# Kernel optimization log

Hardware: AMD Instinct MI355X
Metric: run time of the kernel (lower is better)

The kernel has to match this reference:

```python
import jax, jax.numpy as jnp
import numpy as np
import math

B, N, NBS, E, H = 64, 512, 8, 2048, 128
L, K = 3, 4
AF, BF = 82, 6
NA, NBTAB = 100, 10
ALPHA, LAMDA = 0.1, 0.5


def _gelu(x):
    return jax.nn.gelu(x, approximate=False)


def _mask_softmax(a, mask):
    # a: [..., n], mask broadcastable to a; matches torch mask_softmax (eps=1e-6)
    a_exp = jnp.exp(a - jnp.max(a, -1, keepdims=True)) * mask
    return a_exp / (jnp.sum(a_exp, -1, keepdims=True) + 1e-6)


def _gru(x, h, wih, whh, bih, bhh):
    # torch.nn.GRUCell semantics; wih/whh: [3H, H] in (r, z, n) order
    gi = x @ wih.T + bih
    gh = h @ whh.T + bhh
    ir, iz, inn = jnp.split(gi, 3, -1)
    hr, hz, hn = jnp.split(gh, 3, -1)
    r = jax.nn.sigmoid(ir + hr)
    z = jax.nn.sigmoid(iz + hz)
    n = jnp.tanh(inn + r * hn)
    return (1 - z) * n + z * h


def setup_inputs() -> dict:
    key = jax.random.key(0)
    ks = iter(jax.random.split(key, 64))
    def nrm(shape, s=0.05):
        return jax.random.normal(next(ks), shape, dtype=jnp.float32) * s
    def zb(shape):
        return jnp.zeros(shape, jnp.float32)
    inp = dict(
        batch_size=B,
        vertex_mask=jnp.ones((B, N), jnp.float32),
        vertex=jax.random.randint(next(ks), (B, N), 0, NA),
        edge=jax.random.randint(next(ks), (B, E), 0, NBTAB),
        atom_adj=jax.random.randint(next(ks), (B, N, NBS), 0, B * N),
        bond_adj=jax.random.randint(next(ks), (B, N, NBS), 0, B * E),
        nbs_mask=jnp.ones((B, N, NBS), jnp.float32),
        init_atom_features=nrm((NA, AF), 1.0),
        init_bond_features=nrm((NBTAB, BF), 1.0),
        emb_w=nrm((AF, H)), emb_b=zb((H,)),
        u1_w=nrm((L, H + BF, H)), u1_b=zb((L, H)),
        u2_w=nrm((L, 2 * H, H)), u2_b=zb((L, H)),
        fu_w=nrm((L, H, H)), fu_b=zb((L, H)),
        wvm_w=nrm((L, K, H, H)), wvm_b=zb((L, K, H)),
        wmain_w=nrm((L, K, H, H)), wmain_b=zb((L, K, H)),
        wbmm_w=nrm((L, K, H)), wbmm_b=zb((L, K)),
        khead_w=nrm((L, K * H, H)), khead_b=zb((L, H)),
        wmaster_w=nrm((L, H, H)), wmaster_b=zb((L, H)),
        wm2m_w=nrm((L, H, H)), wm2m_b=zb((L, H)),
        wzm1_w=nrm((L, H, H)), wzm1_b=zb((L, H)),
        wzm2_w=nrm((L, H, H)), wzm2_b=zb((L, H)),
        wzs1_w=nrm((L, H, H)), wzs1_b=zb((L, H)),
        wzs2_w=nrm((L, H, H)), wzs2_b=zb((L, H)),
        gru_main_wih=nrm((3 * H, H)), gru_main_whh=nrm((3 * H, H)),
        gru_main_bih=zb((3 * H,)), gru_main_bhh=zb((3 * H,)),
        gru_master_wih=nrm((3 * H, H)), gru_master_whh=nrm((3 * H, H)),
        gru_master_bih=zb((3 * H,)), gru_master_bhh=zb((3 * H,)),
    )
    return inp


def _compute(p, vertex, edge, atom_adj, bond_adj):
    vm = p['vertex_mask']               # [B, N]
    nm = p['nbs_mask']                  # [B, N, NBS]
    b, n_vertex = vm.shape
    nbs = atom_adj.shape[-1]
    # embed initial atom/bond features via table gather
    v_init = p['init_atom_features'][vertex.reshape(-1)].reshape(b, n_vertex, -1)
    e_init = p['init_bond_features'][edge.reshape(-1)].reshape(b, edge.shape[1], -1)
    v_init = v_init * vm[:, :, None]
    vf = _gelu(v_init @ p['emb_w'] + p['emb_b'])                       # [B, N, H]
    h0 = vf
    hdim = vf.shape[-1]
    master = jnp.sum(vf * vm[:, :, None], axis=1, keepdims=True)        # [B, 1, H]
    aa = atom_adj.reshape(-1)
    ba = bond_adj.reshape(-1)
    n_layers = p['u1_w'].shape[0]
    for i in range(n_layers):
        # --- multi-head main -> master attention (all heads vectorized) ---
        mv = jnp.tanh(jnp.einsum('bnh,khd->bknd', vf, p['wvm_w'][i]) + p['wvm_b'][i][None, :, None, :])
        score = jnp.einsum('bknd,kd->bkn', mv * master[:, None, :, :], p['wbmm_w'][i]) + p['wbmm_b'][i][None, :, None]
        att = _mask_softmax(score, vm[:, None, :])                      # [B, K, N]
        proj = jnp.einsum('bnh,khd->bknd', vf, p['wmain_w'][i]) + p['wmain_b'][i][None, :, None, :]
        kmm = jnp.einsum('bkn,bknd->bkd', att, proj)                    # [B, K, H]
        main_to_master = jnp.tanh(kmm.reshape(b, 1, -1) @ p['khead_w'][i] + p['khead_b'][i])  # [B, 1, H]
        # --- GraphConvolution (dropout p = 0.0) ---
        vn = vf.reshape(-1, hdim)[aa].reshape(b, n_vertex, nbs, hdim)
        en = e_init.reshape(-1, e_init.shape[-1])[ba].reshape(b, n_vertex, nbs, -1)
        lab = _gelu(jnp.concatenate([vn, en], -1) @ p['u1_w'][i] + p['u1_b'][i])
        nl = jnp.sum(lab * nm[..., None], axis=-2)                      # [B, N, H]
        hi = jnp.concatenate([nl, vf], -1) @ p['u2_w'][i] + p['u2_b'][i]
        theta = math.log(LAMDA / (i + 1) + 1)
        support = (1 - ALPHA) * hi + ALPHA * h0
        self_vertex = theta * (support @ p['fu_w'][i] + p['fu_b'][i]) + (1 - theta) * support
        # --- master updates + gated mixing + GRU cells ---
        m2m = _gelu(master @ p['wm2m_w'][i] + p['wm2m_b'][i])           # [B, 1, H]
        mself = _gelu(master @ p['wmaster_w'][i] + p['wmaster_b'][i])   # [B, 1, H]
        z_main = jax.nn.sigmoid(self_vertex @ p['wzm1_w'][i] + p['wzm1_b'][i] + m2m @ p['wzm2_w'][i] + p['wzm2_b'][i])
        hidden_main = (1 - z_main) * self_vertex + z_main * m2m          # broadcast [B,N,H]
        vf = _gru(hidden_main.reshape(-1, hdim), vf.reshape(-1, hdim),
                  p['gru_main_wih'], p['gru_main_whh'], p['gru_main_bih'], p['gru_main_bhh']).reshape(b, n_vertex, hdim)
        z_master = jax.nn.sigmoid(mself @ p['wzs1_w'][i] + p['wzs1_b'][i] + main_to_master @ p['wzs2_w'][i] + p['wzs2_b'][i])
        hidden_super = (1 - z_master) * mself + z_master * main_to_master
        master = _gru(hidden_super.reshape(b, hdim), master.reshape(b, hdim),
                      p['gru_master_wih'], p['gru_master_whh'], p['gru_master_bih'], p['gru_master_bhh']).reshape(b, 1, hdim)
    return vf, master


def reference(batch_size, vertex_mask, vertex, edge, atom_adj, bond_adj, nbs_mask,
              init_atom_features, init_bond_features, emb_w, emb_b,
              u1_w, u1_b, u2_w, u2_b, fu_w, fu_b,
              wvm_w, wvm_b, wmain_w, wmain_b, wbmm_w, wbmm_b, khead_w, khead_b,
              wmaster_w, wmaster_b, wm2m_w, wm2m_b,
              wzm1_w, wzm1_b, wzm2_w, wzm2_b, wzs1_w, wzs1_b, wzs2_w, wzs2_b,
              gru_main_wih, gru_main_whh, gru_main_bih, gru_main_bhh,
              gru_master_wih, gru_master_whh, gru_master_bih, gru_master_bhh):
    p = dict(vertex_mask=vertex_mask, nbs_mask=nbs_mask,
             init_atom_features=init_atom_features, init_bond_features=init_bond_features,
             emb_w=emb_w, emb_b=emb_b, u1_w=u1_w, u1_b=u1_b, u2_w=u2_w, u2_b=u2_b,
             fu_w=fu_w, fu_b=fu_b, wvm_w=wvm_w, wvm_b=wvm_b, wmain_w=wmain_w, wmain_b=wmain_b,
             wbmm_w=wbmm_w, wbmm_b=wbmm_b, khead_w=khead_w, khead_b=khead_b,
             wmaster_w=wmaster_w, wmaster_b=wmaster_b, wm2m_w=wm2m_w, wm2m_b=wm2m_b,
             wzm1_w=wzm1_w, wzm1_b=wzm1_b, wzm2_w=wzm2_w, wzm2_b=wzm2_b,
             wzs1_w=wzs1_w, wzs1_b=wzs1_b, wzs2_w=wzs2_w, wzs2_b=wzs2_b,
             gru_main_wih=gru_main_wih, gru_main_whh=gru_main_whh,
             gru_main_bih=gru_main_bih, gru_main_bhh=gru_main_bhh,
             gru_master_wih=gru_master_wih, gru_master_whh=gru_master_whh,
             gru_master_bih=gru_master_bih, gru_master_bhh=gru_master_bhh)
    return _compute(p, vertex, edge, atom_adj, bond_adj)
```

## Files before the change

kernel.cpp:

```cpp
#include <hip/hip_runtime.h>
#include <hip/hip_bf16.h>
#include <cmath>

#define BB 64
#define NN 512
#define NBS 8
#define EE 2048
#define HH 128
#define LL 3
#define KK 4
#define AF 82
#define BF 6
#define SLAB 4194304

typedef __attribute__((ext_vector_type(8))) short bf16x8;
typedef __attribute__((ext_vector_type(4))) float f32x4;

__device__ __forceinline__ float gelu1(float x){ return 0.5f*x*(1.f+erff(x*0.7071067811865475f)); }
__device__ __forceinline__ float sig1(float x){ return 1.f/(1.f+expf(-x)); }
__device__ __forceinline__ short f2bs(float x){ __hip_bfloat16 b=__float2bfloat16(x); return *reinterpret_cast<short*>(&b); }
__device__ __forceinline__ float bs2f(short s){ unsigned u = ((unsigned)(unsigned short)s) << 16; union{unsigned u; float f;} c; c.u=u; return c.f; }
__device__ __forceinline__ void split2(float v, short& hi, short& lo){ hi = f2bs(v); lo = f2bs(v - bs2f(hi)); }

#define MFMA3(ACC, AH, AL, BH, BL) \
    ACC = __builtin_amdgcn_mfma_f32_16x16x32_bf16(AH, BH, ACC, 0,0,0); \
    ACC = __builtin_amdgcn_mfma_f32_16x16x32_bf16(AL, BH, ACC, 0,0,0); \
    ACC = __builtin_amdgcn_mfma_f32_16x16x32_bf16(AH, BL, ACC, 0,0,0);

__global__ __launch_bounds__(256) void layer_k1(
    const short* __restrict__ vfh, const short* __restrict__ vfl,
    const short* __restrict__ wtpv, short* __restrict__ pvfb,
    const short* __restrict__ wtwvm, const float* __restrict__ wvmb,
    const float* __restrict__ master,
    const float* __restrict__ wbw, const float* __restrict__ wbb,
    float* __restrict__ score)
{
    const int bid = blockIdx.x;
    const int t = threadIdx.x;
    const int lane = t & 63, wv = t >> 6;
    const int quad = lane >> 4, ml = lane & 15;

    if (bid < 256) {
        const int m0 = bid*128 + wv*32;
        const int r0 = m0 + ml, r1 = r0 + 16;

        bf16x8 a0h[4], a0l[4], a1h[4], a1l[4];
        #pragma unroll
        for (int kc = 0; kc < 4; ++kc) {
            const int kq = kc*32 + quad*8;
            a0h[kc] = *(const bf16x8*)(vfh + (size_t)r0*128 + kq);
            a0l[kc] = *(const bf16x8*)(vfl + (size_t)r0*128 + kq);
            a1h[kc] = *(const bf16x8*)(vfh + (size_t)r1*128 + kq);
            a1l[kc] = *(const bf16x8*)(vfl + (size_t)r1*128 + kq);
        }
        f32x4 acc[16];
        #pragma unroll
        for (int i = 0; i < 16; ++i) acc[i] = (f32x4){0.f,0.f,0.f,0.f};
        const short* wcol = wtpv + (size_t)ml*128;
        #pragma unroll
        for (int kc = 0; kc < 4; ++kc) {
            const int kq = kc*32 + quad*8;
            #pragma unroll
            for (int nt = 0; nt < 8; ++nt) {
                const short* bp = wcol + (size_t)nt*16*128 + kq;
                bf16x8 bh = *(const bf16x8*)bp;
                bf16x8 bl = *(const bf16x8*)(bp + 49152);
                MFMA3(acc[nt],   a0h[kc], a0l[kc], bh, bl);
                MFMA3(acc[8+nt], a1h[kc], a1l[kc], bh, bl);
            }
        }
        #pragma unroll
        for (int mt = 0; mt < 2; ++mt)
            #pragma unroll
            for (int nt = 0; nt < 8; ++nt) {
                int col = nt*16 + ml;
                #pragma unroll
                for (int r = 0; r < 4; ++r) {
                    int gm = m0 + mt*16 + quad*4 + r;
                    pvfb[(size_t)gm*128 + col] = f2bs(acc[mt*8+nt][r]);
                }
            }
    } else {
        const int v = bid - 256;
        const int k = v >> 8;
        const int tile = v & 255;
        const int b = tile >> 2;
        const int r0 = tile*128 + wv*32 + ml;
        const int r1 = r0 + 16;

        bf16x8 a0h[4], a0l[4], a1h[4], a1l[4];
        #pragma unroll
        for (int kc = 0; kc < 4; ++kc) {
            const int kq = kc*32 + quad*8;
            a0h[kc] = *(const bf16x8*)(vfh + (size_t)r0*128 + kq);
            a0l[kc] = *(const bf16x8*)(vfl + (size_t)r0*128 + kq);
            a1h[kc] = *(const bf16x8*)(vfh + (size_t)r1*128 + kq);
            a1l[kc] = *(const bf16x8*)(vfl + (size_t)r1*128 + kq);
        }
        f32x4 acc[16];
        #pragma unroll
        for (int i = 0; i < 16; ++i) acc[i] = (f32x4){0.f,0.f,0.f,0.f};
        const short* wcol = wtwvm + (size_t)k*16384 + (size_t)ml*128;
        #pragma unroll
        for (int kc = 0; kc < 4; ++kc) {
            const int kq = kc*32 + quad*8;
            #pragma unroll
            for (int nt = 0; nt < 8; ++nt) {
                const short* bp = wcol + (size_t)nt*16*128 + kq;
                bf16x8 bh = *(const bf16x8*)bp;
                bf16x8 bl = *(const bf16x8*)(bp + 196608);
                MFMA3(acc[nt],   a0h[kc], a0l[kc], bh, bl);
                MFMA3(acc[8+nt], a1h[kc], a1l[kc], bh, bl);
            }
        }
        float wv8[8], bj8[8];
        #pragma unroll
        for (int nt = 0; nt < 8; ++nt) {
            int col = nt*16 + ml;
            wv8[nt] = master[(size_t)b*128 + col] * wbw[(size_t)k*128 + col];
            bj8[nt] = wvmb[(size_t)k*128 + col];
        }
        float kb = wbb[k];
        #pragma unroll
        for (int mt = 0; mt < 2; ++mt) {
            #pragma unroll
            for (int r = 0; r < 4; ++r) {
                float s = 0.f;
                #pragma unroll
                for (int nt = 0; nt < 8; ++nt)
                    s += tanhf(acc[mt*8+nt][r] + bj8[nt]) * wv8[nt];
                s += __shfl_xor(s, 1); s += __shfl_xor(s, 2);
                s += __shfl_xor(s, 4); s += __shfl_xor(s, 8);
                if (ml == 0) {
                    int nloc = (tile & 3)*128 + wv*32 + mt*16 + quad*4 + r;
                    score[((size_t)(b*KK + k))*NN + nloc] = s + kb;
                }
            }
        }
    }
}

__global__ __launch_bounds__(256) void layer_k2(
    const short* __restrict__ pvfb, const float* __restrict__ pet,
    const int* __restrict__ aadj, const int* __restrict__ badj,
    const int* __restrict__ edge, const float* __restrict__ nbm,
    short* __restrict__ nlh, short* __restrict__ nll,
    const float* __restrict__ score, const float* __restrict__ vm,
    const float* __restrict__ vfc,
    float* __restrict__ satt, float* __restrict__ ctx)
{
    __shared__ float smem[768];
    const int bid = blockIdx.x;
    const int t = threadIdx.x;

    if (bid < 8192) {
        const int w = t >> 6, l = t & 63;
        const int i = bid*4 + w;
        const int sg = l >> 4, j = l & 15;
        float acc[8];
        #pragma unroll
        for (int c = 0; c < 8; ++c) acc[c] = 0.f;
        #pragma unroll
        for (int it = 0; it < 2; ++it) {
            int s = it*4 + sg;
            int flat = i*8 + s;
            int g = aadj[flat];
            int eid = edge[badj[flat]];
            float nv = nbm[flat];
            bf16x8 pv8 = *(const bf16x8*)(pvfb + (size_t)g*128 + j*8);
            const float* pp = pet + (size_t)eid*128 + j*8;
            float4 p0 = *(const float4*)pp, p1 = *(const float4*)(pp+4);
            float pe[8] = {p0.x,p0.y,p0.z,p0.w,p1.x,p1.y,p1.z,p1.w};
            #pragma unroll
            for (int c = 0; c < 8; ++c)
                acc[c] += gelu1(bs2f(pv8[c]) + pe[c]) * nv;
        }
        #pragma unroll
        for (int c = 0; c < 8; ++c) {
            acc[c] += __shfl_xor(acc[c], 16);
            acc[c] += __shfl_xor(acc[c], 32);
        }
        if (sg == 0) {
            short hs[8], ls[8];
            #pragma unroll
            for (int c = 0; c < 8; ++c) split2(acc[c], hs[c], ls[c]);
            size_t o = (size_t)i*128 + j*8;
            *(short4*)(nlh + o)     = make_short4(hs[0],hs[1],hs[2],hs[3]);
            *(short4*)(nlh + o + 4) = make_short4(hs[4],hs[5],hs[6],hs[7]);
            *(short4*)(nll + o)     = make_short4(ls[0],ls[1],ls[2],ls[3]);
            *(short4*)(nll + o + 4) = make_short4(ls[4],ls[5],ls[6],ls[7]);
        }
    } else {
        float* red = smem;
        float* att = smem + 256;
        const int bk = bid - 8192, b = bk >> 2;
        float v0 = score[(size_t)bk*NN + t], v1 = score[(size_t)bk*NN + 256 + t];
        red[t] = fmaxf(v0, v1); __syncthreads();
        for (int s = 128; s; s >>= 1) { if (t < s) red[t] = fmaxf(red[t], red[t+s]); __syncthreads(); }
        float mx = red[0]; __syncthreads();
        float e0 = expf(v0 - mx) * vm[b*NN + t];
        float e1 = expf(v1 - mx) * vm[b*NN + t + 256];
        red[t] = e0 + e1; __syncthreads();
        for (int s = 128; s; s >>= 1) { if (t < s) red[t] += red[t+s]; __syncthreads(); }
        float sum = red[0];
        float inv = 1.f / (sum + 1e-6f);
        att[t] = e0*inv; att[t+256] = e1*inv;
        if (t == 0) satt[bk] = sum*inv;
        __syncthreads();
        const int d = t & 127, h = t >> 7;
        float acc = 0.f;
        const float* V = vfc + (size_t)b*NN*HH;
        #pragma unroll 8
        for (int n = h*256; n < h*256 + 256; ++n) acc += att[n]*V[(size_t)n*HH + d];
        red[t] = acc; __syncthreads();
        if (t < 128) ctx[(size_t)bk*HH + t] = red[t] + red[t+128];
    }
}

__global__ __launch_bounds__(256, 2) void layer_k3(
    const short* __restrict__ nlh, const short* __restrict__ nll,
    const float* __restrict__ vfc, const short* __restrict__ vfch, const short* __restrict__ vfcl,
    float* __restrict__ vfn, short* __restrict__ vfnh, short* __restrict__ vfnl,
    const short* __restrict__ h0b,
    const short* __restrict__ wu2, const float* __restrict__ u2b,
    const short* __restrict__ wfu, const float* __restrict__ fub,
    const short* __restrict__ wzm, const float* __restrict__ zmb,
    const short* __restrict__ wih, const short* __restrict__ whh,
    const float* __restrict__ bih, const float* __restrict__ bhh,
    const float* __restrict__ t2, const float* __restrict__ m2m,
    float theta,
    const float* __restrict__ ctx, const float* __restrict__ satt,
    float* __restrict__ master,
    const float* __restrict__ wmain_w, const float* __restrict__ wmain_b,
    const float* __restrict__ khead_w, const float* __restrict__ khead_b,
    const float* __restrict__ wmaster_w, const float* __restrict__ wmaster_b,
    const float* __restrict__ wzs1_w,  const float* __restrict__ wzs1_b,
    const float* __restrict__ wzs2_w,  const float* __restrict__ wzs2_b,
    const float* __restrict__ WTih, const float* __restrict__ WThh,
    const float* __restrict__ bihm, const float* __restrict__ bhhm,
    const float* __restrict__ wm2m_n_w, const float* __restrict__ wm2m_n_b,
    const float* __restrict__ wzm2_n_w, const float* __restrict__ wzm2_n_b,
    float* __restrict__ m2m_out, float* __restrict__ t2_out)
{
    __shared__ __align__(16) char smem_raw[34816];
    const int bid = blockIdx.x;
    const int t = threadIdx.x;

    if (bid >= 64) {
        short* sh = (short*)smem_raw;
        short* sl = sh + 64*136;
        const int vb = bid - 64;
        const int lane = t & 63, wv = t >> 6;
        const int quad = lane >> 4, ml = lane & 15;
        const int base = vb * 64;
        const int bb = base >> 9;
        const int c0 = wv*32 + ml;
        const int c1 = c0 + 16;
        const int kq0 = quad*8;

        f32x4 acc[4][2];
        #pragma unroll
        for (int rt = 0; rt < 4; ++rt) {
            acc[rt][0] = (f32x4){0.f,0.f,0.f,0.f};
            acc[rt][1] = (f32x4){0.f,0.f,0.f,0.f};
        }

        #pragma unroll
        for (int kc = 0; kc < 4; ++kc) {
            const int kq = kc*32 + kq0;
            const short* bp0 = wu2 + (size_t)c0*256 + kq;
            const short* bp1 = wu2 + (size_t)c1*256 + kq;
            bf16x8 b0h = *(const bf16x8*)bp0, b0l = *(const bf16x8*)(bp0+98304);
            bf16x8 b1h = *(const bf16x8*)bp1, b1l = *(const bf16x8*)(bp1+98304);
            #pragma unroll
            for (int rt = 0; rt < 4; ++rt) {
                const size_t ar = (size_t)(base + rt*16 + ml);
                bf16x8 ah = *(const bf16x8*)(nlh + ar*128 + kq);
                bf16x8 al = *(const bf16x8*)(nll + ar*128 + kq);
                MFMA3(acc[rt][0], ah, al, b0h, b0l);
                MFMA3(acc[rt][1], ah, al, b1h, b1l);
            }
        }
        #pragma unroll
        for (int kc = 0; kc < 4; ++kc) {
            const int kq = kc*32 + kq0;
            const short* bp0 = wu2 + (size_t)c0*256 + 128 + kq;
            const short* bp1 = wu2 + (size_t)c1*256 + 128 + kq;
            bf16x8 b0h = *(const bf16x8*)bp0, b0l = *(const bf16x8*)(bp0+98304);
            bf16x8 b1h = *(const bf16x8*)bp1, b1l = *(const bf16x8*)(bp1+98304);
            #pragma unroll
            for (int rt = 0; rt < 4; ++rt) {
                const size_t ar = (size_t)(base + rt*16 + ml);
                bf16x8 ah = *(const bf16x8*)(vfch + ar*128 + kq);
                bf16x8 al = *(const bf16x8*)(vfcl + ar*128 + kq);
                MFMA3(acc[rt][0], ah, al, b0h, b0l);
                MFMA3(acc[rt][1], ah, al, b1h, b1l);
            }
        }
        f32x4 sup[4][2];
        {
            const float bj0 = u2b[c0], bj1 = u2b[c1];
            #pragma unroll
            for (int rt = 0; rt < 4; ++rt) {
                #pragma unroll
                for (int r = 0; r < 4; ++r) {
                    const size_t grow = (size_t)(base + rt*16 + quad*4 + r);
                    sup[rt][0][r] = 0.9f*(acc[rt][0][r]+bj0) + 0.1f*bs2f(h0b[grow*128 + c0]);
                    sup[rt][1][r] = 0.9f*(acc[rt][1][r]+bj1) + 0.1f*bs2f(h0b[grow*128 + c1]);
                    const int lrow = rt*16 + quad*4 + r;
                    short h_, l_;
                    split2(sup[rt][0][r], h_, l_); sh[lrow*136 + c0] = h_; sl[lrow*136 + c0] = l_;
                    split2(sup[rt][1][r], h_, l_); sh[lrow*136 + c1] = h_; sl[lrow*136 + c1] = l_;
                }
            }
        }
        __syncthreads();

        #pragma unroll
        for (int rt = 0; rt < 4; ++rt) {
            acc[rt][0] = (f32x4){0.f,0.f,0.f,0.f};
            acc[rt][1] = (f32x4){0.f,0.f,0.f,0.f};
        }
        #pragma unroll
        for (int kc = 0; kc < 4; ++kc) {
            const int kq = kc*32 + kq0;
            const short* bp0 = wfu + (size_t)c0*128 + kq;
            const short* bp1 = wfu + (size_t)c1*128 + kq;
            bf16x8 b0h = *(const bf16x8*)bp0, b0l = *(const bf16x8*)(bp0+49152);
            bf16x8 b1h = *(const bf16x8*)bp1, b1l = *(const bf16x8*)(bp1+49152);
            #pragma unroll
            for (int rt = 0; rt < 4; ++rt) {
                bf16x8 xh = *(const bf16x8*)&sh[(rt*16+ml)*136 + kq];
                bf16x8 xl = *(const bf16x8*)&sl[(rt*16+ml)*136 + kq];
                MFMA3(acc[rt][0], xh, xl, b0h, b0l);
                MFMA3(acc[rt][1], xh, xl, b1h, b1l);
            }
        }
        f32x4 sv[4][2];
        {
            const float bj0 = fub[c0], bj1 = fub[c1];
            #pragma unroll
            for (int rt = 0; rt < 4; ++rt) {
                #pragma unroll
                for (int r = 0; r < 4; ++r) {
                    sv[rt][0][r] = theta*(acc[rt][0][r]+bj0) + (1.f-theta)*sup[rt][0][r];
                    sv[rt][1][r] = theta*(acc[rt][1][r]+bj1) + (1.f-theta)*sup[rt][1][r];
                }
            }
        }
        __syncthreads();
        #pragma unroll
        for (int rt = 0; rt < 4; ++rt) {
            #pragma unroll
            for (int r = 0; r < 4; ++r) {
                const int lrow = rt*16 + quad*4 + r;
                short h_, l_;
                split2(sv[rt][0][r], h_, l_); sh[lrow*136 + c0] = h_; sl[lrow*136 + c0] = l_;
                split2(sv[rt][1][r], h_, l_); sh[lrow*136 + c1] = h_; sl[lrow*136 + c1] = l_;
            }
        }
        __syncthreads();

        #pragma unroll
        for (int rt = 0; rt < 4; ++rt) {
            acc[rt][0] = (f32x4){0.f,0.f,0.f,0.f};
            acc[rt][1] = (f32x4){0.f,0.f,0.f,0.f};
        }
        #pragma unroll
        for (int kc = 0; kc < 4; ++kc) {
            const int kq = kc*32 + kq0;
            const short* bp0 = wzm + (size_t)c0*128 + kq;
            const short* bp1 = wzm + (size_t)c1*128 + kq;
            bf16x8 b0h = *(const bf16x8*)bp0, b0l = *(const bf16x8*)(bp0+49152);
            bf16x8 b1h = *(const bf16x8*)bp1, b1l = *(const bf16x8*)(bp1+49152);
            #pragma unroll
            for (int rt = 0; rt < 4; ++rt) {
                bf16x8 xh = *(const bf16x8*)&sh[(rt*16+ml)*136 + kq];
                bf16x8 xl = *(const bf16x8*)&sl[(rt*16+ml)*136 + kq];
                MFMA3(acc[rt][0], xh, xl, b0h, b0l);
                MFMA3(acc[rt][1], xh, xl, b1h, b1l);
            }
        }
        f32x4 hid[4][2];
        {
            const float bj0 = zmb[c0], bj1 = zmb[c1];
            const float t20 = t2[(size_t)bb*128 + c0], t21 = t2[(size_t)bb*128 + c1];
            const float m20 = m2m[(size_t)bb*128 + c0], m21 = m2m[(size_t)bb*128 + c1];
            #pragma unroll
            for (int rt = 0; rt < 4; ++rt) {
                #pragma unroll
                for (int r = 0; r < 4; ++r) {
                    float z0 = sig1(acc[rt][0][r] + bj0 + t20);
                    float z1 = sig1(acc[rt][1][r] + bj1 + t21);
                    hid[rt][0][r] = (1.f-z0)*sv[rt][0][r] + z0*m20;
                    hid[rt][1][r] = (1.f-z1)*sv[rt][1][r] + z1*m21;
                }
            }
        }
        __syncthreads();
        #pragma unroll
        for (int rt = 0; rt < 4; ++rt) {
            #pragma unroll
            for (int r = 0; r < 4; ++r) {
                const int lrow = rt*16 + quad*4 + r;
                short h_, l_;
                split2(hid[rt][0][r], h_, l_); sh[lrow*136 + c0] = h_; sl[lrow*136 + c0] = l_;
                split2(hid[rt][1][r], h_, l_); sh[lrow*136 + c1] = h_; sl[lrow*136 + c1] = l_;
            }
        }
        __syncthreads();

        f32x4 gr[4][2], gi[4][2], gh[4][2];
        #pragma unroll
        for (int rt = 0; rt < 4; ++rt) {
            gr[rt][0] = (f32x4){0.f,0.f,0.f,0.f};
            gr[rt][1] = (f32x4){0.f,0.f,0.f,0.f};
        }
        #pragma unroll
        for (int kc = 0; kc < 4; ++kc) {
            const int kq = kc*32 + kq0;
            const short* pw0 = wih + (size_t)c0*128 + kq;
            const short* pw1 = wih + (size_t)c1*128 + kq;
            const short* pu0 = whh + (size_t)c0*128 + kq;
            const short* pu1 = whh + (size_t)c1*128 + kq;
            bf16x8 w0h=*(const bf16x8*)pw0, w0l=*(const bf16x8*)(pw0+49152);
            bf16x8 w1h=*(const bf16x8*)pw1, w1l=*(const bf16x8*)(pw1+49152);
            bf16x8 u0h=*(const bf16x8*)pu0, u0l=*(const bf16x8*)(pu0+49152);
            bf16x8 u1h=*(const bf16x8*)pu1, u1l=*(const bf16x8*)(pu1+49152);
            #pragma unroll
            for (int rt = 0; rt < 4; ++rt) {
                const size_t ar = (size_t)(base + rt*16 + ml);
                bf16x8 xh = *(const bf16x8*)&sh[(rt*16+ml)*136 + kq];
                bf16x8 xl = *(const bf16x8*)&sl[(rt*16+ml)*136 + kq];
                bf16x8 hh = *(const bf16x8*)(vfch + ar*128 + kq);
                bf16x8 hl = *(const bf16x8*)(vfcl + ar*128 + kq);
                MFMA3(gr[rt][0], xh, xl, w0h, w0l);
                MFMA3(gr[rt][0], hh, hl, u0h, u0l);
                MFMA3(gr[rt][1], xh, xl, w1h, w1l);
                MFMA3(gr[rt][1], hh, hl, u1h, u1l);
            }
        }
        {
            const float br0 = bih[c0] + bhh[c0], br1 = bih[c1] + bhh[c1];
            #pragma unroll
            for (int rt = 0; rt < 4; ++rt) {
                #pragma unroll
                for (int r = 0; r < 4; ++r) {
                    gr[rt][0][r] = sig1(gr[rt][0][r] + br0);
                    gr[rt][1][r] = sig1(gr[rt][1][r] + br1);
                }
            }
        }
        #pragma unroll
        for (int rt = 0; rt < 4; ++rt) {
            gi[rt][0] = (f32x4){0.f,0.f,0.f,0.f};
            gi[rt][1] = (f32x4){0.f,0.f,0.f,0.f};
            gh[rt][0] = (f32x4){0.f,0.f,0.f,0.f};
            gh[rt][1] = (f32x4){0.f,0.f,0.f,0.f};
        }
        #pragma unroll
        for (int kc = 0; kc < 4; ++kc) {
            const int kq = kc*32 + kq0;
            const short* pw0 = wih + (size_t)(256 + c0)*128 + kq;
            const short* pw1 = wih + (size_t)(256 + c1)*128 + kq;
            const short* pu0 = whh + (size_t)(256 + c0)*128 + kq;
            const short* pu1 = whh + (size_t)(256 + c1)*128 + kq;
            bf16x8 w0h=*(const bf16x8*)pw0, w0l=*(const bf16x8*)(pw0+49152);
            bf16x8 w1h=*(const bf16x8*)pw1, w1l=*(const bf16x8*)(pw1+49152);
            bf16x8 u0h=*(const bf16x8*)pu0, u0l=*(const bf16x8*)(pu0+49152);
            bf16x8 u1h=*(const bf16x8*)pu1, u1l=*(const bf16x8*)(pu1+49152);
            #pragma unroll
            for (int rt = 0; rt < 4; ++rt) {
                const size_t ar = (size_t)(base + rt*16 + ml);
                bf16x8 xh = *(const bf16x8*)&sh[(rt*16+ml)*136 + kq];
                bf16x8 xl = *(const bf16x8*)&sl[(rt*16+ml)*136 + kq];
                bf16x8 hh = *(const bf16x8*)(vfch + ar*128 + kq);
                bf16x8 hl = *(const bf16x8*)(vfcl + ar*128 + kq);
                MFMA3(gi[rt][0], xh, xl, w0h, w0l);
                MFMA3(gh[rt][0], hh, hl, u0h, u0l);
                MFMA3(gi[rt][1], xh, xl, w1h, w1l);
                MFMA3(gh[rt][1], hh, hl, u1h, u1l);
            }
        }
        {
            const float bn0 = bih[256+c0], bn1 = bih[256+c1];
            const float un0 = bhh[256+c0], un1 = bhh[256+c1];
            #pragma unroll
            for (int rt = 0; rt < 4; ++rt) {
                #pragma unroll
                for (int r = 0; r < 4; ++r) {
                    gi[rt][0][r] = tanhf(gi[rt][0][r] + bn0 + gr[rt][0][r]*(gh[rt][0][r] + un0));
                    gi[rt][1][r] = tanhf(gi[rt][1][r] + bn1 + gr[rt][1][r]*(gh[rt][1][r] + un1));
                }
            }
        }
        #pragma unroll
        for (int rt = 0; rt < 4; ++rt) {
            gh[rt][0] = (f32x4){0.f,0.f,0.f,0.f};
            gh[rt][1] = (f32x4){0.f,0.f,0.f,0.f};
        }
        #pragma unroll
        for (int kc = 0; kc < 4; ++kc) {
            const int kq = kc*32 + kq0;
            const short* pw0 = wih + (size_t)(128 + c0)*128 + kq;
            const short* pw1 = wih + (size_t)(128 + c1)*128 + kq;
            const short* pu0 = whh + (size_t)(128 + c0)*128 + kq;
            const short* pu1 = whh + (size_t)(128 + c1)*128 + kq;
            bf16x8 w0h=*(const bf16x8*)pw0, w0l=*(const bf16x8*)(pw0+49152);
            bf16x8 w1h=*(const bf16x8*)pw1, w1l=*(const bf16x8*)(pw1+49152);
            bf16x8 u0h=*(const bf16x8*)pu0, u0l=*(const bf16x8*)(pu0+49152);
            bf16x8 u1h=*(const bf16x8*)pu1, u1l=*(const bf16x8*)(pu1+49152);
            #pragma unroll
            for (int rt = 0; rt < 4; ++rt) {
                const size_t ar = (size_t)(base + rt*16 + ml);
                bf16x8 xh = *(const bf16x8*)&sh[(rt*16+ml)*136 + kq];
                bf16x8 xl = *(const bf16x8*)&sl[(rt*16+ml)*136 + kq];
                bf16x8 hh = *(const bf16x8*)(vfch + ar*128 + kq);
                bf16x8 hl = *(const bf16x8*)(vfcl + ar*128 + kq);
                MFMA3(gh[rt][0], xh, xl, w0h, w0l);
                MFMA3(gh[rt][0], hh, hl, u0h, u0l);
                MFMA3(gh[rt][1], xh, xl, w1h, w1l);
                MFMA3(gh[rt][1], hh, hl, u1h, u1l);
            }
        }
        {
            const float bz0 = bih[128+c0] + bhh[128+c0];
            const float bz1 = bih[128+c1] + bhh[128+c1];
            #pragma unroll
            for (int rt = 0; rt < 4; ++rt) {
                #pragma unroll
                for (int r = 0; r < 4; ++r) {
                    const size_t grow = (size_t)(base + rt*16 + quad*4 + r);
                    const size_t off0 = grow*128 + c0, off1 = grow*128 + c1;
                    float z0 = sig1(gh[rt][0][r] + bz0);
                    float z1 = sig1(gh[rt][1][r] + bz1);
                    float o0 = (1.f-z0)*gi[rt][0][r] + z0*vfc[off0];
                    float o1 = (1.f-z1)*gi[rt][1][r] + z1*vfc[off1];
                    vfn[off0] = o0; vfn[off1] = o1;
                    short h_, l_;
                    split2(o0, h_, l_); vfnh[off0] = h_; vfnl[off0] = l_;
                    split2(o1, h_, l_); vfnh[off1] = h_; vfnl[off1] = l_;
                }
            }
        }
    } else {
        float* smemf = (float*)smem_raw;
        float* xs = smemf;
        float* ms = smemf + 512;
        float* msN = smemf + 640;
        float* v_mtm = smemf + 768;
        float* v_mself = smemf + 896;
        float* v_m2m = smemf + 1024;
        float* v_t2 = smemf + 1152;
        float* v_ts1 = smemf + 1280;
        float* v_ts2 = smemf + 1408;
        float* v_hsup = smemf + 1536;
        float* gi = smemf + 1664;
        float* gh2 = smemf + 2048;
        float* red = smemf + 2432;
        const int b = bid;

        if (t < 128) ms[t] = master[(size_t)b*128 + t];
        __syncthreads();

        const int c = t & 127, p = t >> 7;

        #pragma unroll
        for (int k = 0; k < 4; ++k) {
            const float* cx = ctx + ((size_t)b*KK + k)*128;
            const float* Wk = wmain_w + (size_t)k*16384;
            float s = 0.f;
            for (int d = p*64; d < p*64+64; ++d) s += cx[d]*Wk[(size_t)d*128 + c];
            red[t] = s; __syncthreads();
            if (t < 128) xs[k*128 + c] = red[c] + red[c+128] + satt[(size_t)b*KK + k]*wmain_b[k*128 + c];
            __syncthreads();
        }

        auto matvec = [&](const float* src, const float* __restrict__ W,
                          const float* __restrict__ bias, int K, float* out, int act) {
            int half = K >> 1;
            int k0 = p*half, k1 = k0 + half;
            float s = 0.f;
            for (int k = k0; k < k1; ++k) s += src[k]*W[(size_t)k*128 + c];
            red[t] = s; __syncthreads();
            if (t < 128) {
                float v = red[c] + red[c+128] + bias[c];
                if (act == 1) v = gelu1(v); else if (act == 2) v = tanhf(v);
                out[c] = v;
            }
            __syncthreads();
        };

        matvec(xs, khead_w, khead_b, 512, v_mtm, 2);
        matvec(ms, wmaster_w, wmaster_b, 128, v_mself, 1);
        matvec(v_mself, wzs1_w, wzs1_b, 128, v_ts1, 0);
        matvec(v_mtm, wzs2_w, wzs2_b, 128, v_ts2, 0);

        if (t < 128) {
            float z = sig1(v_ts1[t] + v_ts2[t]);
            v_hsup[t] = (1.f-z)*v_mself[t] + z*v_mtm[t];
        }
        __syncthreads();

        for (int j = t; j < 384; j += 256) {
            float a = 0.f, h2 = 0.f;
            for (int k = 0; k < 128; ++k) {
                a  += v_hsup[k]*WTih[(size_t)k*384 + j];
                h2 += ms[k]*WThh[(size_t)k*384 + j];
            }
            gi[j] = a + bihm[j];
            gh2[j] = h2 + bhhm[j];
        }
        __syncthreads();
        if (t < 128) {
            float r = sig1(gi[t] + gh2[t]);
            float z = sig1(gi[128+t] + gh2[128+t]);
            float n = tanhf(gi[256+t] + r*gh2[256+t]);
            float nm = (1.f-z)*n + z*ms[t];
            master[(size_t)b*128 + t] = nm;
            msN[t] = nm;
        }
        __syncthreads();

        matvec(msN, wm2m_n_w, wm2m_n_b, 128, v_m2m, 1);
        matvec(v_m2m, wzm2_n_w, wzm2_n_b, 128, v_t2, 0);
        if (t < 128) {
            m2m_out[(size_t)b*128 + t] = v_m2m[t];
            t2_out[(size_t)b*128 + t]  = v_t2[t];
        }
    }
}

__global__ __launch_bounds__(256) void embed_kernel(
    const float* __restrict__ atomf, const int* __restrict__ vertex,
    const float* __restrict__ vmask,
    const short* __restrict__ WT, const float* __restrict__ bias,
    float* __restrict__ vf, short* __restrict__ h0b,
    short* __restrict__ vfh, short* __restrict__ vfl)
{
    const int t = threadIdx.x;
    const int lane = t & 63, wv = t >> 6;
    const int quad = lane >> 4, ml = lane & 15;
    const int m0 = blockIdx.x*128 + wv*32;
    const int r0 = m0 + ml, r1 = m0 + 16 + ml;
    const int ga0 = vertex[r0], ga1 = vertex[r1];
    const float vm0 = vmask[r0], vm1 = vmask[r1];

    f32x4 acc[16];
    #pragma unroll
    for (int i = 0; i < 16; ++i) acc[i] = (f32x4){0.f,0.f,0.f,0.f};
    const short* wcol = WT + (size_t)ml*96;

    #pragma unroll
    for (int kc = 0; kc < 3; ++kc) {
        const int kq = kc*32 + quad*8;
        float av0[8], av1[8];
        const float* p0r = atomf + (size_t)ga0*AF + kq;
        const float* p1r = atomf + (size_t)ga1*AF + kq;
        #pragma unroll
        for (int j2 = 0; j2 < 4; ++j2) {
            int k = kq + 2*j2;
            if (k + 2 <= AF) {
                float2 v0 = *(const float2*)(p0r + 2*j2);
                float2 v1 = *(const float2*)(p1r + 2*j2);
                av0[2*j2]=v0.x*vm0; av0[2*j2+1]=v0.y*vm0;
                av1[2*j2]=v1.x*vm1; av1[2*j2+1]=v1.y*vm1;
            } else { av0[2*j2]=0.f; av0[2*j2+1]=0.f; av1[2*j2]=0.f; av1[2*j2+1]=0.f; }
        }
        bf16x8 a0h, a0l, a1h, a1l;
        #pragma unroll
        for (int j = 0; j < 8; ++j) {
            short h, l;
            split2(av0[j], h, l); a0h[j]=h; a0l[j]=l;
            split2(av1[j], h, l); a1h[j]=h; a1l[j]=l;
        }
        #pragma unroll
        for (int nt = 0; nt < 8; ++nt) {
            const short* bp = wcol + (size_t)nt*16*96 + kq;
            bf16x8 bh = *(const bf16x8*)bp;
            bf16x8 bl = *(const bf16x8*)(bp + 12288);
            MFMA3(acc[nt],   a0h, a0l, bh, bl);
            MFMA3(acc[8+nt], a1h, a1l, bh, bl);
        }
    }

    #pragma unroll
    for (int mt = 0; mt < 2; ++mt) {
        #pragma unroll
        for (int nt = 0; nt < 8; ++nt) {
            int col = nt*16 + ml;
            float bj = bias[col];
            #pragma unroll
            for (int r = 0; r < 4; ++r) {
                int gm = m0 + mt*16 + quad*4 + r;
                float v = gelu1(acc[mt*8+nt][r] + bj);
                size_t off = (size_t)gm*128 + col;
                vf[off] = v;
                short h_, l_; split2(v, h_, l_);
                vfh[off] = h_; vfl[off] = l_;
                h0b[off] = h_;
            }
        }
    }
}

__global__ __launch_bounds__(256) void master_init2(
    const float* __restrict__ vf, const float* __restrict__ vm,
    const float* __restrict__ wm2m_w, const float* __restrict__ wm2m_b,
    const float* __restrict__ wzm2_w, const float* __restrict__ wzm2_b,
    float* __restrict__ master, float* __restrict__ m2m_out, float* __restrict__ t2_out)
{
    __shared__ float red[256], ms[128], v_m2m[128];
    const int b = blockIdx.x, t = threadIdx.x;
    const int hcol = t & 127, half = t >> 7;
    float s = 0.f;
    for (int n = half; n < NN; n += 2)
        s += vf[((size_t)b*NN + n)*HH + hcol] * vm[b*NN + n];
    red[t] = s; __syncthreads();
    if (half == 0) { float v = red[hcol] + red[hcol+128]; ms[hcol] = v; master[(size_t)b*HH + hcol] = v; }
    __syncthreads();
    const int c = t & 127, p = t >> 7;
    {
        float s2 = 0.f;
        for (int k = p*64; k < p*64+64; ++k) s2 += ms[k]*wm2m_w[(size_t)k*128 + c];
        red[t] = s2; __syncthreads();
        if (t < 128) { float v = gelu1(red[c] + red[c+128] + wm2m_b[c]); v_m2m[c] = v; m2m_out[(size_t)b*128 + c] = v; }
        __syncthreads();
    }
    {
        float s2 = 0.f;
        for (int k = p*64; k < p*64+64; ++k) s2 += v_m2m[k]*wzm2_w[(size_t)k*128 + c];
        red[t] = s2; __syncthreads();
        if (t < 128) t2_out[(size_t)b*128 + c] = red[c] + red[c+128] + wzm2_b[c];
    }
}

__device__ __forceinline__ void cvt_t2(const float* __restrict__ src, short* __restrict__ dst,
                                       int i, int K, int Kpad, int total, int zrows)
{
    int z = i / (128*Kpad); int rem = i - z*128*Kpad;
    int col = rem / Kpad; int k = rem - col*Kpad;
    float v = (k < K) ? src[(size_t)z*zrows*128 + (size_t)k*128 + col] : 0.f;
    short h, l; split2(v, h, l);
    dst[i] = h; dst[total + i] = l;
}

__global__ void wprep_kernel(
    const float* __restrict__ emb_w, const float* __restrict__ wvm_w,
    const float* __restrict__ u1_w, const float* __restrict__ u1_b,
    const float* __restrict__ u2_w,
    const float* __restrict__ fu_w, const float* __restrict__ wzm1_w,
    const float* __restrict__ g_wih, const float* __restrict__ g_whh,
    const float* __restrict__ gm_wih, const float* __restrict__ gm_whh,
    const float* __restrict__ bondf,
    short* __restrict__ wt_emb, short* __restrict__ wt_wvm,
    short* __restrict__ wt_pv, short* __restrict__ wt_u2,
    short* __restrict__ wt_fu, short* __restrict__ wt_wzm1,
    short* __restrict__ wt_gih, short* __restrict__ wt_ghh,
    float* __restrict__ WTih_s, float* __restrict__ WThh_s,
    float* __restrict__ pet)
{
    int i = blockIdx.x*256 + threadIdx.x;
    if (i < 12288) cvt_t2(emb_w, wt_emb, i, 82, 96, 12288, 82);
    else if (i < 208896) cvt_t2(wvm_w, wt_wvm, i-12288, 128, 128, 196608, 128);
    else if (i < 258048) cvt_t2(u1_w, wt_pv, i-208896, 128, 128, 49152, 134);
    else if (i < 356352) cvt_t2(u2_w, wt_u2, i-258048, 256, 256, 98304, 256);
    else if (i < 405504) cvt_t2(fu_w, wt_fu, i-356352, 128, 128, 49152, 128);
    else if (i < 454656) cvt_t2(wzm1_w, wt_wzm1, i-405504, 128, 128, 49152, 128);
    else if (i < 503808) { int j = i-454656; short h,l; split2(g_wih[j],h,l); wt_gih[j]=h; wt_gih[49152+j]=l; }
    else if (i < 552960) { int j = i-503808; short h,l; split2(g_whh[j],h,l); wt_ghh[j]=h; wt_ghh[49152+j]=l; }
    else if (i < 602112) { int o = i-552960; int k = o/384, j = o-k*384; WTih_s[o] = gm_wih[j*128 + k]; }
    else if (i < 651264) { int o = i-602112; int k = o/384, j = o-k*384; WThh_s[o] = gm_whh[j*128 + k]; }
    else if (i < 655104) {
        int o = i-651264;
        int l = o / 1280; int rem = o - l*1280;
        int e = rem >> 7; int c = rem & 127;
        float acc = u1_b[l*128 + c];
        #pragma unroll
        for (int j = 0; j < 6; ++j)
            acc += bondf[e*6 + j] * u1_w[((size_t)l*134 + 128 + j)*128 + c];
        pet[o] = acc;
    }
}

__global__ void copy_out_kernel(const float* __restrict__ vf, const float* __restrict__ master,
                                float* __restrict__ out)
{
    int i = blockIdx.x*256 + threadIdx.x;
    const int nvf4 = SLAB/4;
    if (i < nvf4) ((float4*)out)[i] = ((const float4*)vf)[i];
    else ((float4*)out)[i] = ((const float4*)master)[i - nvf4];
}

extern "C" void kernel_launch(void* const* d_in, const int* in_sizes, int n_in,
                              void* d_out, int out_size, void* d_ws, size_t ws_size,
                              hipStream_t stream)
{
    (void)in_sizes; (void)n_in; (void)out_size; (void)ws_size;
    const float* vmask = (const float*)d_in[1];
    const int*   vertex= (const int*)d_in[2];
    const int*   edge  = (const int*)d_in[3];
    const int*   aadj  = (const int*)d_in[4];
    const int*   badj  = (const int*)d_in[5];
    const float* nbm   = (const float*)d_in[6];
    const float* atomf = (const float*)d_in[7];
    const float* bondf = (const float*)d_in[8];
    const float* emb_w = (const float*)d_in[9];
    const float* emb_b = (const float*)d_in[10];
    const float* u1_w  = (const float*)d_in[11];
    const float* u1_b  = (const float*)d_in[12];
    const float* u2_w  = (const float*)d_in[13];
    const float* u2_b  = (const float*)d_in[14];
    const float* fu_w  = (const float*)d_in[15];
    const float* fu_b  = (const float*)d_in[16];
    const float* wvm_w = (const float*)d_in[17];
    const float* wvm_b = (const float*)d_in[18];
    const float* wmain_w=(const float*)d_in[19];
    const float* wmain_b=(const float*)d_in[20];
    const float* wbmm_w= (const float*)d_in[21];
    const float* wbmm_b= (const float*)d_in[22];
    const float* khead_w=(const float*)d_in[23];
    const float* khead_b=(const float*)d_in[24];
    const float* wmaster_w=(const float*)d_in[25];
    const float* wmaster_b=(const float*)d_in[26];
    const float* wm2m_w= (const float*)d_in[27];
    const float* wm2m_b= (const float*)d_in[28];
    const float* wzm1_w= (const float*)d_in[29];
    const float* wzm1_b= (const float*)d_in[30];
    const float* wzm2_w= (const float*)d_in[31];
    const float* wzm2_b= (const float*)d_in[32];
    const float* wzs1_w= (const float*)d_in[33];
    const float* wzs1_b= (const float*)d_in[34];
    const float* wzs2_w= (const float*)d_in[35];
    const float* wzs2_b= (const float*)d_in[36];
    const float* g_wih = (const float*)d_in[37];
    const float* g_whh = (const float*)d_in[38];
    const float* g_bih = (const float*)d_in[39];
    const float* g_bhh = (const float*)d_in[40];
    const float* gm_wih= (const float*)d_in[41];
    const float* gm_whh= (const float*)d_in[42];
    const float* gm_bih= (const float*)d_in[43];
    const float* gm_bhh= (const float*)d_in[44];

    float* ws     = (float*)d_ws;
    float* vfA    = ws;
    float* vfB    = vfA + SLAB;
    float* score  = vfB + SLAB;
    float* ctx    = score + BB*KK*NN;
    float* satt   = ctx + BB*KK*HH;
    float* master = satt + BB*KK;
    float* m2mA   = master + BB*HH;
    float* t2A    = m2mA + BB*HH;
    float* m2mB   = t2A + BB*HH;
    float* t2B    = m2mB + BB*HH;
    float* WTih_s = t2B + BB*HH;
    float* WThh_s = WTih_s + 128*384;
    float* pet    = WThh_s + 128*384;
    short* vfhA   = (short*)(pet + 3840);
    short* vflA   = vfhA + SLAB;
    short* vfhB   = vflA + SLAB;
    short* vflB   = vfhB + SLAB;
    short* nlh    = vflB + SLAB;
    short* nll    = nlh + SLAB;
    short* pvfb   = nll + SLAB;
    short* h0b    = pvfb + SLAB;
    short* wt_emb   = h0b + SLAB;
    short* wt_wvm   = wt_emb   + 2*12288;
    short* wt_pv    = wt_wvm   + 2*196608;
    short* wt_u2    = wt_pv    + 2*49152;
    short* wt_fu    = wt_u2    + 2*98304;
    short* wt_wzm1  = wt_fu    + 2*49152;
    short* wt_gih   = wt_wzm1  + 2*49152;
    short* wt_ghh   = wt_gih   + 2*49152;

    wprep_kernel<<<2560, 256, 0, stream>>>(
        emb_w, wvm_w, u1_w, u1_b, u2_w, fu_w, wzm1_w, g_wih, g_whh, gm_wih, gm_whh,
        bondf,
        wt_emb, wt_wvm, wt_pv, wt_u2, wt_fu, wt_wzm1, wt_gih, wt_ghh,
        WTih_s, WThh_s, pet);

    embed_kernel<<<256, 256, 0, stream>>>(atomf, vertex, vmask, wt_emb, emb_b,
                                          vfA, h0b, vfhA, vflA);

    master_init2<<<BB, 256, 0, stream>>>(vfA, vmask, wm2m_w, wm2m_b, wzm2_w, wzm2_b,
                                         master, m2mA, t2A);

    for (int i = 0; i < LL; ++i) {
        float theta = logf(0.5f/(float)(i+1) + 1.f);
        const bool even = (i % 2 == 0);
        float* vfc  = even ? vfA  : vfB;
        short* vfch = even ? vfhA : vfhB;
        short* vfcl = even ? vflA : vflB;
        float* vfn  = even ? vfB  : vfA;
        short* vfnh = even ? vfhB : vfhA;
        short* vfnl = even ? vflB : vflA;
        float* m2mR = even ? m2mA : m2mB;
        float* t2R  = even ? t2A  : t2B;
        float* m2mW = even ? m2mB : m2mA;
        float* t2W  = even ? t2B  : t2A;
        int nx = (i+1 < LL) ? i+1 : i;

        layer_k1<<<1280, 256, 0, stream>>>(
            vfch, vfcl,
            wt_pv + (size_t)i*16384, pvfb,
            wt_wvm + (size_t)i*4*16384, wvm_b + (size_t)i*4*128,
            master, wbmm_w + (size_t)i*KK*HH, wbmm_b + (size_t)i*KK, score);

        layer_k2<<<8448, 256, 0, stream>>>(
            pvfb, pet + (size_t)i*1280,
            aadj, badj, edge, nbm, nlh, nll,
            score, vmask, vfc, satt, ctx);

        layer_k3<<<576, 256, 0, stream>>>(
            nlh, nll, vfc, vfch, vfcl, vfn, vfnh, vfnl, h0b,
            wt_u2 + (size_t)i*128*256, u2_b + i*HH,
            wt_fu + (size_t)i*16384, fu_b + i*HH,
            wt_wzm1 + (size_t)i*16384, wzm1_b + i*HH,
            wt_gih, wt_ghh, g_bih, g_bhh,
            t2R, m2mR, theta,
            ctx, satt, master,
            wmain_w + (size_t)i*KK*HH*HH, wmain_b + (size_t)i*KK*HH,
            khead_w + (size_t)i*KK*HH*HH, khead_b + i*HH,
            wmaster_w + (size_t)i*HH*HH, wmaster_b + i*HH,
            wzs1_w + (size_t)i*HH*HH, wzs1_b + i*HH,
            wzs2_w + (size_t)i*HH*HH, wzs2_b + i*HH,
            WTih_s, WThh_s, gm_bih, gm_bhh,
            wm2m_w + (size_t)nx*HH*HH, wm2m_b + nx*HH,
            wzm2_w + (size_t)nx*HH*HH, wzm2_b + nx*HH,
            m2mW, t2W);
    }

    copy_out_kernel<<<(SLAB + BB*HH)/4/256, 256, 0, stream>>>(vfB, master, (float*)d_out);
}
```

Before: 831.0 us.

## Fold fu and wzm1 GEMMs into parallel combined weight; split master init

```diff
diff --git a/kernel.cpp b/kernel.cpp
--- a/kernel.cpp
+++ b/kernel.cpp
@@ -224,7 +224,7 @@
     const short* __restrict__ h0b,
     const short* __restrict__ wu2, const float* __restrict__ u2b,
     const short* __restrict__ wfu, const float* __restrict__ fub,
-    const short* __restrict__ wzm, const float* __restrict__ zmb,
+    const short* __restrict__ wbc, const float* __restrict__ zmb2v,
     const short* __restrict__ wih, const short* __restrict__ whh,
     const float* __restrict__ bih, const float* __restrict__ bhh,
     const float* __restrict__ t2, const float* __restrict__ m2m,
@@ -316,84 +316,51 @@
         }
         __syncthreads();
 
+        f32x4 accz[4][2];
         #pragma unroll
         for (int rt = 0; rt < 4; ++rt) {
             acc[rt][0] = (f32x4){0.f,0.f,0.f,0.f};
             acc[rt][1] = (f32x4){0.f,0.f,0.f,0.f};
+            accz[rt][0] = (f32x4){0.f,0.f,0.f,0.f};
+            accz[rt][1] = (f32x4){0.f,0.f,0.f,0.f};
         }
         #pragma unroll
         for (int kc = 0; kc < 4; ++kc) {
             const int kq = kc*32 + kq0;
             const short* bp0 = wfu + (size_t)c0*128 + kq;
             const short* bp1 = wfu + (size_t)c1*128 + kq;
+            const short* zp0 = wbc + (size_t)c0*128 + kq;
+            const short* zp1 = wbc + (size_t)c1*128 + kq;
             bf16x8 b0h = *(const bf16x8*)bp0, b0l = *(const bf16x8*)(bp0+49152);
             bf16x8 b1h = *(const bf16x8*)bp1, b1l = *(const bf16x8*)(bp1+49152);
+            bf16x8 z0h = *(const bf16x8*)zp0, z0l = *(const bf16x8*)(zp0+49152);
+            bf16x8 z1h = *(const bf16x8*)zp1, z1l = *(const bf16x8*)(zp1+49152);
             #pragma unroll
             for (int rt = 0; rt < 4; ++rt) {
                 bf16x8 xh = *(const bf16x8*)&sh[(rt*16+ml)*136 + kq];
                 bf16x8 xl = *(const bf16x8*)&sl[(rt*16+ml)*136 + kq];
                 MFMA3(acc[rt][0], xh, xl, b0h, b0l);
                 MFMA3(acc[rt][1], xh, xl, b1h, b1l);
-            }
-        }
-        f32x4 sv[4][2];
+                MFMA3(accz[rt][0], xh, xl, z0h, z0l);
+                MFMA3(accz[rt][1], xh, xl, z1h, z1l);
+            }
+        }
+        f32x4 hid[4][2];
         {
             const float bj0 = fub[c0], bj1 = fub[c1];
+            const float zb0 = zmb2v[c0] + t2[(size_t)bb*128 + c0];
+            const float zb1 = zmb2v[c1] + t2[(size_t)bb*128 + c1];
+            const float m20 = m2m[(size_t)bb*128 + c0], m21 = m2m[(size_t)bb*128 + c1];
             #pragma unroll
             for (int rt = 0; rt < 4; ++rt) {
                 #pragma unroll
                 for (int r = 0; r < 4; ++r) {
-                    sv[rt][0][r] = theta*(acc[rt][0][r]+bj0) + (1.f-theta)*sup[rt][0][r];
-                    sv[rt][1][r] = theta*(acc[rt][1][r]+bj1) + (1.f-theta)*sup[rt][1][r];
-                }
-            }
-        }
-        __syncthreads();
-        #pragma unroll
-        for (int rt = 0; rt < 4; ++rt) {
-            #pragma unroll
-            for (int r = 0; r < 4; ++r) {
-                const int lrow = rt*16 + quad*4 + r;
-                short h_, l_;
-                split2(sv[rt][0][r], h_, l_); sh[lrow*136 + c0] = h_; sl[lrow*136 + c0] = l_;
-                split2(sv[rt][1][r], h_, l_); sh[lrow*136 + c1] = h_; sl[lrow*136 + c1] = l_;
-            }
-        }
-        __syncthreads();
-
-        #pragma unroll
-        for (int rt = 0; rt < 4; ++rt) {
-            acc[rt][0] = (f32x4){0.f,0.f,0.f,0.f};
-            acc[rt][1] = (f32x4){0.f,0.f,0.f,0.f};
-        }
-        #pragma unroll
-        for (int kc = 0; kc < 4; ++kc) {
-            const int kq = kc*32 + kq0;
-            const short* bp0 = wzm + (size_t)c0*128 + kq;
-            const short* bp1 = wzm + (size_t)c1*128 + kq;
-            bf16x8 b0h = *(const bf16x8*)bp0, b0l = *(const bf16x8*)(bp0+49152);
-            bf16x8 b1h = *(const bf16x8*)bp1, b1l = *(const bf16x8*)(bp1+49152);
-            #pragma unroll
-            for (int rt = 0; rt < 4; ++rt) {
-                bf16x8 xh = *(const bf16x8*)&sh[(rt*16+ml)*136 + kq];
-                bf16x8 xl = *(const bf16x8*)&sl[(rt*16+ml)*136 + kq];
-                MFMA3(acc[rt][0], xh, xl, b0h, b0l);
-                MFMA3(acc[rt][1], xh, xl, b1h, b1l);
-            }
-        }
-        f32x4 hid[4][2];
-        {
-            const float bj0 = zmb[c0], bj1 = zmb[c1];
-            const float t20 = t2[(size_t)bb*128 + c0], t21 = t2[(size_t)bb*128 + c1];
-            const float m20 = m2m[(size_t)bb*128 + c0], m21 = m2m[(size_t)bb*128 + c1];
-            #pragma unroll
-            for (int rt = 0; rt < 4; ++rt) {
-                #pragma unroll
-                for (int r = 0; r < 4; ++r) {
-                    float z0 = sig1(acc[rt][0][r] + bj0 + t20);
-                    float z1 = sig1(acc[rt][1][r] + bj1 + t21);
-                    hid[rt][0][r] = (1.f-z0)*sv[rt][0][r] + z0*m20;
-                    hid[rt][1][r] = (1.f-z1)*sv[rt][1][r] + z1*m21;
+                    float sv0 = theta*(acc[rt][0][r]+bj0) + (1.f-theta)*sup[rt][0][r];
+                    float sv1 = theta*(acc[rt][1][r]+bj1) + (1.f-theta)*sup[rt][1][r];
+                    float z0 = sig1(accz[rt][0][r] + zb0);
+                    float z1 = sig1(accz[rt][1][r] + zb1);
+                    hid[rt][0][r] = (1.f-z0)*sv0 + z0*m20;
+                    hid[rt][1][r] = (1.f-z1)*sv1 + z1*m21;
                 }
             }
         }
@@ -704,20 +671,31 @@
     }
 }
 
-__global__ __launch_bounds__(256) void master_init2(
+__global__ __launch_bounds__(256) void master_init_a(
     const float* __restrict__ vf, const float* __restrict__ vm,
+    float* __restrict__ master)
+{
+    __shared__ float red[256];
+    const int bid = blockIdx.x;
+    const int b = bid >> 3, sl = bid & 7;
+    const int t = threadIdx.x;
+    const int c = t & 127, half = t >> 7;
+    float s = 0.f;
+    for (int n = sl*64 + half; n < sl*64 + 64; n += 2)
+        s += vf[((size_t)b*NN + n)*HH + c] * vm[b*NN + n];
+    red[t] = s; __syncthreads();
+    if (t < 128) atomicAdd(&master[(size_t)b*HH + c], red[c] + red[c+128]);
+}
+
+__global__ __launch_bounds__(256) void master_init_b(
+    const float* __restrict__ master,
     const float* __restrict__ wm2m_w, const float* __restrict__ wm2m_b,
     const float* __restrict__ wzm2_w, const float* __restrict__ wzm2_b,
-    float* __restrict__ master, float* __restrict__ m2m_out, float* __restrict__ t2_out)
+    float* __restrict__ m2m_out, float* __restrict__ t2_out)
 {
     __shared__ float red[256], ms[128], v_m2m[128];
     const int b = blockIdx.x, t = threadIdx.x;
-    const int hcol = t & 127, half = t >> 7;
-    float s = 0.f;
-    for (int n = half; n < NN; n += 2)
-        s += vf[((size_t)b*NN + n)*HH + hcol] * vm[b*NN + n];
-    red[t] = s; __syncthreads();
-    if (half == 0) { float v = red[hcol] + red[hcol+128]; ms[hcol] = v; master[(size_t)b*HH + hcol] = v; }
+    if (t < 128) ms[t] = master[(size_t)b*HH + t];
     __syncthreads();
     const int c = t & 127, p = t >> 7;
     {
@@ -749,7 +727,8 @@
     const float* __restrict__ emb_w, const float* __restrict__ wvm_w,
     const float* __restrict__ u1_w, const float* __restrict__ u1_b,
     const float* __restrict__ u2_w,
-    const float* __restrict__ fu_w, const float* __restrict__ wzm1_w,
+    const float* __restrict__ fu_w, const float* __restrict__ fu_bv,
+    const float* __restrict__ wzm1_w, const float* __restrict__ wzm1_bv,
     const float* __restrict__ g_wih, const float* __restrict__ g_whh,
     const float* __restrict__ gm_wih, const float* __restrict__ gm_whh,
     const float* __restrict__ bondf,
@@ -757,8 +736,9 @@
     short* __restrict__ wt_pv, short* __restrict__ wt_u2,
     short* __restrict__ wt_fu, short* __restrict__ wt_wzm1,
     short* __restrict__ wt_gih, short* __restrict__ wt_ghh,
+    short* __restrict__ wt_wbc, float* __restrict__ zmb2,
     float* __restrict__ WTih_s, float* __restrict__ WThh_s,
-    float* __restrict__ pet)
+    float* __restrict__ pet, float* __restrict__ master0)
 {
     int i = blockIdx.x*256 + threadIdx.x;
     if (i < 12288) cvt_t2(emb_w, wt_emb, i, 82, 96, 12288, 82);
@@ -780,6 +760,31 @@
         for (int j = 0; j < 6; ++j)
             acc += bondf[e*6 + j] * u1_w[((size_t)l*134 + 128 + j)*128 + c];
         pet[o] = acc;
+    }
+    else if (i < 704256) {
+        int o = i - 655104;
+        int li = o >> 14; int rem = o & 16383;
+        int k = rem >> 7; int c = rem & 127;
+        float theta = logf(0.5f/(float)(li+1) + 1.f);
+        const float* fu = fu_w + (size_t)li*16384 + (size_t)k*128;
+        const float* wz = wzm1_w + (size_t)li*16384;
+        float s = 0.f;
+        for (int j = 0; j < 128; ++j) s += fu[j] * wz[(size_t)j*128 + c];
+        s = theta*s + (1.f-theta)*wz[(size_t)k*128 + c];
+        short h, lo; split2(s, h, lo);
+        size_t d = (size_t)li*16384 + (size_t)c*128 + k;
+        wt_wbc[d] = h; wt_wbc[49152 + d] = lo;
+    }
+    else if (i < 704640) {
+        int o = i - 704256; int li = o >> 7; int c = o & 127;
+        float theta = logf(0.5f/(float)(li+1) + 1.f);
+        float s = 0.f;
+        for (int j = 0; j < 128; ++j)
+            s += fu_bv[li*128 + j] * wzm1_w[(size_t)li*16384 + (size_t)j*128 + c];
+        zmb2[o] = wzm1_bv[li*128 + c] + theta*s;
+    }
+    else if (i < 712832) {
+        master0[i - 704640] = 0.f;
     }
 }
 
@@ -872,18 +877,21 @@
     short* wt_wzm1  = wt_fu    + 2*49152;
     short* wt_gih   = wt_wzm1  + 2*49152;
     short* wt_ghh   = wt_gih   + 2*49152;
-
-    wprep_kernel<<<2560, 256, 0, stream>>>(
-        emb_w, wvm_w, u1_w, u1_b, u2_w, fu_w, wzm1_w, g_wih, g_whh, gm_wih, gm_whh,
-        bondf,
+    short* wt_wbc   = wt_ghh   + 2*49152;
+    float* zmb2     = (float*)(wt_wbc + 2*49152);
+
+    wprep_kernel<<<2785, 256, 0, stream>>>(
+        emb_w, wvm_w, u1_w, u1_b, u2_w, fu_w, fu_b, wzm1_w, wzm1_b,
+        g_wih, g_whh, gm_wih, gm_whh, bondf,
         wt_emb, wt_wvm, wt_pv, wt_u2, wt_fu, wt_wzm1, wt_gih, wt_ghh,
-        WTih_s, WThh_s, pet);
+        wt_wbc, zmb2, WTih_s, WThh_s, pet, master);
 
     embed_kernel<<<256, 256, 0, stream>>>(atomf, vertex, vmask, wt_emb, emb_b,
                                           vfA, h0b, vfhA, vflA);
 
-    master_init2<<<BB, 256, 0, stream>>>(vfA, vmask, wm2m_w, wm2m_b, wzm2_w, wzm2_b,
-                                         master, m2mA, t2A);
+    master_init_a<<<512, 256, 0, stream>>>(vfA, vmask, master);
+    master_init_b<<<BB, 256, 0, stream>>>(master, wm2m_w, wm2m_b, wzm2_w, wzm2_b,
+                                          m2mA, t2A);
 
     for (int i = 0; i < LL; ++i) {
         float theta = logf(0.5f/(float)(i+1) + 1.f);
@@ -915,7 +923,7 @@
             nlh, nll, vfc, vfch, vfcl, vfn, vfnh, vfnl, h0b,
             wt_u2 + (size_t)i*128*256, u2_b + i*HH,
             wt_fu + (size_t)i*16384, fu_b + i*HH,
-            wt_wzm1 + (size_t)i*16384, wzm1_b + i*HH,
+            wt_wbc + (size_t)i*16384, zmb2 + i*HH,
             wt_gih, wt_ghh, g_bih, g_bhh,
             t2R, m2mR, theta,
             ctx, satt, master,
```

Result: faster. 783.0 us (-5.8%).
